# Kernel optimization log

Hardware: AMD Instinct MI355X
Metric: run time of the kernel (lower is better)

The kernel has to match this reference:

```python
import jax, jax.numpy as jnp
import numpy as np

EPS = 0.1

def _kernels():
    # torch: sobel = [[-0.5,0,0.5]]*3 (2D), repeated along depth -> [1,1,3,3,3]
    s = np.array([[-0.5, 0.0, 0.5]] * 3, dtype=np.float32)        # grad along W
    kx = np.tile(s[None, :, :], (3, 1, 1))                        # [3,3,3]
    ky = np.tile(s.T[None, :, :], (3, 1, 1))                      # grad along H
    kz = np.zeros((3, 3, 3), dtype=np.float32)
    kz[0, :, :] = -0.5
    kz[2, :, :] = 0.5                                             # grad along D
    # OIDHW, O=I=1 (channel=1 depthwise)
    return (jnp.asarray(kx)[None, None], jnp.asarray(ky)[None, None], jnp.asarray(kz)[None, None])

KX, KY, KZ = _kernels()

def _conv(x, k):
    return jax.lax.conv_general_dilated(
        x, k, window_strides=(1, 1, 1), padding='VALID',
        dimension_numbers=('NCDHW', 'OIDHW', 'NCDHW'))

def _grads(x):
    # ReplicationPad3d(1) == edge padding on D,H,W
    xp = jnp.pad(x, ((0, 0), (0, 0), (1, 1), (1, 1), (1, 1)), mode='edge')
    return _conv(xp, KX), _conv(xp, KY), _conv(xp, KZ)

def setup_inputs() -> dict:
    key = jax.random.key(0)
    k1, k2, k3 = jax.random.split(key, 3)
    shp = (1, 1, 192, 192, 192)
    return {
        'I': jax.random.normal(k1, shp, dtype=jnp.float32),
        'J': jax.random.normal(k2, shp, dtype=jnp.float32),
        'mask': jax.random.uniform(k3, shp, dtype=jnp.float32),
    }

def reference(I, J, mask):
    Ix, Iy, Iz = _grads(I)
    Jx, Jy, Jz = _grads(J)
    I_mag = Ix * Ix + Iy * Iy + Iz * Iz + EPS * EPS
    J_mag = Jx * Jx + Jy * Jy + Jz * Jz + EPS * EPS
    dot = Ix * Jx + Iy * Jy + Iz * Jz          # == sum over concat channel dim (C=1)
    ngf = (dot * dot) / (I_mag * J_mag)
    return jnp.mean((1.0 - ngf) * mask)
```

## Files before the change

kernel.cpp:

```cpp
#include <hip/hip_runtime.h>

#define NN 192
#define BZ 4
#define YC 8
#define NTHR (64 * BZ)


__device__ __forceinline__ void row_ab(float c0, float c1, float c2, int lane,
                                       float a[3], float b[3]) {
    float L = __shfl_up(c2, 1, 64);
    float R = __shfl_down(c0, 1, 64);
    if (lane == 0)  L = c0;
    if (lane == 63) R = c2;
    a[0] = c1 - L;
    a[1] = c2 - c0;
    a[2] = R - c1;
    b[0] = L + c0 + c1;
    b[1] = c0 + c1 + c2;
    b[2] = c1 + c2 + R;
}

__device__ __forceinline__ void fold_plane(const float3 r[3], int lane,
                                           float sa[3], float sb[3], float tb[3]) {
    float am[3], bm[3], a0[3], b0[3], ap[3], bp[3];
    row_ab(r[0].x, r[0].y, r[0].z, lane, am, bm);
    row_ab(r[1].x, r[1].y, r[1].z, lane, a0, b0);
    row_ab(r[2].x, r[2].y, r[2].z, lane, ap, bp);
#pragma unroll
    for (int i = 0; i < 3; ++i) {
        sa[i] = am[i] + a0[i] + ap[i];
        sb[i] = bm[i] + b0[i] + bp[i];
        tb[i] = bp[i] - bm[i];
    }
}

__device__ __forceinline__ void load_plane(const float* const base[6], int yrow,
                                           float3 rI[3], float3 rJ[3]) {
#pragma unroll
    for (int d = 0; d < 3; ++d) rI[d] = *reinterpret_cast<const float3*>(base[d] + yrow);
#pragma unroll
    for (int d = 0; d < 3; ++d) rJ[d] = *reinterpret_cast<const float3*>(base[3 + d] + yrow);
}

__global__ __launch_bounds__(NTHR, 2) void ngf_kernel(const float* __restrict__ I,
                                                      const float* __restrict__ J,
                                                      const float* __restrict__ M,
                                                      float* __restrict__ out) {
    const int lane = threadIdx.x;
    const int tz = threadIdx.y;
    const int xoff = lane * 3;
    const int z = blockIdx.y * BZ + tz;
    const int ybase = blockIdx.x * YC;

    const int gzm = (z == 0) ? 0 : z - 1;
    const int gzp = (z == NN - 1) ? (NN - 1) : z + 1;

    const float* base[6] = {
        I + gzm * NN * NN + xoff, I + z * NN * NN + xoff, I + gzp * NN * NN + xoff,
        J + gzm * NN * NN + xoff, J + z * NN * NN + xoff, J + gzp * NN * NN + xoff};
    const float* mbase = M + z * NN * NN + xoff;

    float sa[2][3][3], sb[2][3][3], tb[2][3][3];

    {
        float3 rI[3], rJ[3];
        load_plane(base, ((ybase == 0) ? 0 : (ybase - 1)) * NN, rI, rJ);
        fold_plane(rI, lane, sa[0][0], sb[0][0], tb[0][0]);
        fold_plane(rJ, lane, sa[1][0], sb[1][0], tb[1][0]);
        load_plane(base, ybase * NN, rI, rJ);
        fold_plane(rI, lane, sa[0][1], sb[0][1], tb[0][1]);
        fold_plane(rJ, lane, sa[1][1], sb[1][1], tb[1][1]);
    }

    float3 bI[2][3], bJ[2][3];
    load_plane(base, (ybase + 1) * NN, bI[0], bJ[0]);
    float3 mcur = *reinterpret_cast<const float3*>(mbase + ybase * NN);

    float acc = 0.0f;
#pragma unroll
    for (int yy = 0; yy < YC; ++yy) {
        const int cb = yy & 1, nb = cb ^ 1;

        float3 mnxt = mcur;
        if (yy < YC - 1) {
            int gy = ybase + yy + 2;
            gy = (gy > NN - 1) ? (NN - 1) : gy;
            load_plane(base, gy * NN, bI[nb], bJ[nb]);
            mnxt = *reinterpret_cast<const float3*>(mbase + (ybase + yy + 1) * NN);
        }

        const int sC = (yy + 2) % 3;
        fold_plane(bI[cb], lane, sa[0][sC], sb[0][sC], tb[0][sC]);
        fold_plane(bJ[cb], lane, sa[1][sC], sb[1][sC], tb[1][sC]);

        const int s0 = yy % 3, s1 = (yy + 1) % 3;
        const float mm[3] = {mcur.x, mcur.y, mcur.z};
#pragma unroll
        for (int i = 0; i < 3; ++i) {
            const float Ix = sa[0][s0][i] + sa[0][s1][i] + sa[0][sC][i];
            const float Iy = sb[0][sC][i] - sb[0][s0][i];
            const float Iz = tb[0][s0][i] + tb[0][s1][i] + tb[0][sC][i];
            const float Jx = sa[1][s0][i] + sa[1][s1][i] + sa[1][sC][i];
            const float Jy = sb[1][sC][i] - sb[1][s0][i];
            const float Jz = tb[1][s0][i] + tb[1][s1][i] + tb[1][sC][i];
            const float im = Ix * Ix + Iy * Iy + Iz * Iz + 0.04f;
            const float jm = Jx * Jx + Jy * Jy + Jz * Jz + 0.04f;
            const float dot = Ix * Jx + Iy * Jy + Iz * Jz;
            acc += (1.0f - dot * dot * __builtin_amdgcn_rcpf(im * jm)) * mm[i];
        }
        mcur = mnxt;
    }

    acc *= (1.0f / ((float)NN * (float)NN * (float)NN));
#pragma unroll
    for (int off = 32; off > 0; off >>= 1)
        acc += __shfl_down(acc, off, 64);

    __shared__ float red[NTHR / 64];
    const int flat = tz * 64 + lane;
    if ((flat & 63) == 0) red[flat >> 6] = acc;
    __syncthreads();
    if (flat == 0) {
        float s = 0.0f;
#pragma unroll
        for (int w = 0; w < NTHR / 64; ++w) s += red[w];
        atomicAdd(out, s);
    }
}

extern "C" void kernel_launch(void* const* d_in, const int* in_sizes, int n_in,
                              void* d_out, int out_size, void* d_ws, size_t ws_size,
                              hipStream_t stream) {
    const float* I = (const float*)d_in[0];
    const float* J = (const float*)d_in[1];
    const float* M = (const float*)d_in[2];
    float* out = (float*)d_out;

    hipMemsetAsync(d_out, 0, sizeof(float), stream);

    dim3 block(64, BZ);
    dim3 grid(NN / YC, NN / BZ);
    ngf_kernel<<<grid, block, 0, stream>>>(I, J, M, out);
}
```

Measured before the change: 118.4 us.

## Refactor separable gradient folding to shuffle depth-reduced sums and enlarge y chunk

Restructures the separable stencil so each plane first reduces along depth (sum and difference), then exchanges only those two partials across lanes. That cuts cross-lane shuffles from six per row-triple to four, and the x, y and z gradients are assembled from 5-wide S/D/T windows. It also raises the per-block y chunk from 8 to 12 rows, which amortizes halo reloads, and asks for occupancy of 3 blocks per CU. The larger windows and chunk raise register pressure, which could force spills under the tighter launch bound, and with YC=12 the grid has fewer blocks.

Result: slower. 121.7 us (+2.7%).

```diff
diff --git a/kernel.cpp b/kernel.cpp
--- a/kernel.cpp
+++ b/kernel.cpp
@@ -2,36 +2,26 @@
 
 #define NN 192
 #define BZ 4
-#define YC 8
+#define YC 12
 #define NTHR (64 * BZ)
 
 
-__device__ __forceinline__ void row_ab(float c0, float c1, float c2, int lane,
-                                       float a[3], float b[3]) {
-    float L = __shfl_up(c2, 1, 64);
-    float R = __shfl_down(c0, 1, 64);
-    if (lane == 0)  L = c0;
-    if (lane == 63) R = c2;
-    a[0] = c1 - L;
-    a[1] = c2 - c0;
-    a[2] = R - c1;
-    b[0] = L + c0 + c1;
-    b[1] = c0 + c1 + c2;
-    b[2] = c1 + c2 + R;
-}
-
-__device__ __forceinline__ void fold_plane(const float3 r[3], int lane,
-                                           float sa[3], float sb[3], float tb[3]) {
-    float am[3], bm[3], a0[3], b0[3], ap[3], bp[3];
-    row_ab(r[0].x, r[0].y, r[0].z, lane, am, bm);
-    row_ab(r[1].x, r[1].y, r[1].z, lane, a0, b0);
-    row_ab(r[2].x, r[2].y, r[2].z, lane, ap, bp);
-#pragma unroll
-    for (int i = 0; i < 3; ++i) {
-        sa[i] = am[i] + a0[i] + ap[i];
-        sb[i] = bm[i] + b0[i] + bp[i];
-        tb[i] = bp[i] - bm[i];
-    }
+__device__ __forceinline__ void fold_pq(const float3 rm, const float3 r0, const float3 rp,
+                                        int lane, float pe[5], float qe[5]) {
+    const float p0 = rm.x + r0.x + rp.x;
+    const float p1 = rm.y + r0.y + rp.y;
+    const float p2 = rm.z + r0.z + rp.z;
+    const float q0 = rp.x - rm.x;
+    const float q1 = rp.y - rm.y;
+    const float q2 = rp.z - rm.z;
+    float pL = __shfl_up(p2, 1, 64);
+    float pR = __shfl_down(p0, 1, 64);
+    float qL = __shfl_up(q2, 1, 64);
+    float qR = __shfl_down(q0, 1, 64);
+    if (lane == 0)  { pL = p0; qL = q0; }
+    if (lane == 63) { pR = p2; qR = q2; }
+    pe[0] = pL; pe[1] = p0; pe[2] = p1; pe[3] = p2; pe[4] = pR;
+    qe[0] = qL; qe[1] = q0; qe[2] = q1; qe[3] = q2; qe[4] = qR;
 }
 
 __device__ __forceinline__ void load_plane(const float* const base[6], int yrow,
@@ -42,7 +32,7 @@
     for (int d = 0; d < 3; ++d) rJ[d] = *reinterpret_cast<const float3*>(base[3 + d] + yrow);
 }
 
-__global__ __launch_bounds__(NTHR, 2) void ngf_kernel(const float* __restrict__ I,
+__global__ __launch_bounds__(NTHR, 3) void ngf_kernel(const float* __restrict__ I,
                                                       const float* __restrict__ J,
                                                       const float* __restrict__ M,
                                                       float* __restrict__ out) {
@@ -60,16 +50,16 @@
         J + gzm * NN * NN + xoff, J + z * NN * NN + xoff, J + gzp * NN * NN + xoff};
     const float* mbase = M + z * NN * NN + xoff;
 
-    float sa[2][3][3], sb[2][3][3], tb[2][3][3];
+    float pe[2][3][5], qe[2][3][5];
 
     {
         float3 rI[3], rJ[3];
         load_plane(base, ((ybase == 0) ? 0 : (ybase - 1)) * NN, rI, rJ);
-        fold_plane(rI, lane, sa[0][0], sb[0][0], tb[0][0]);
-        fold_plane(rJ, lane, sa[1][0], sb[1][0], tb[1][0]);
+        fold_pq(rI[0], rI[1], rI[2], lane, pe[0][0], qe[0][0]);
+        fold_pq(rJ[0], rJ[1], rJ[2], lane, pe[1][0], qe[1][0]);
         load_plane(base, ybase * NN, rI, rJ);
-        fold_plane(rI, lane, sa[0][1], sb[0][1], tb[0][1]);
-        fold_plane(rJ, lane, sa[1][1], sb[1][1], tb[1][1]);
+        fold_pq(rI[0], rI[1], rI[2], lane, pe[0][1], qe[0][1]);
+        fold_pq(rJ[0], rJ[1], rJ[2], lane, pe[1][1], qe[1][1]);
     }
 
     float3 bI[2][3], bJ[2][3];
@@ -90,19 +80,32 @@
         }
 
         const int sC = (yy + 2) % 3;
-        fold_plane(bI[cb], lane, sa[0][sC], sb[0][sC], tb[0][sC]);
-        fold_plane(bJ[cb], lane, sa[1][sC], sb[1][sC], tb[1][sC]);
+        fold_pq(bI[cb][0], bI[cb][1], bI[cb][2], lane, pe[0][sC], qe[0][sC]);
+        fold_pq(bJ[cb][0], bJ[cb][1], bJ[cb][2], lane, pe[1][sC], qe[1][sC]);
 
         const int s0 = yy % 3, s1 = (yy + 1) % 3;
+        float G[2][3][3];
+#pragma unroll
+        for (int ar = 0; ar < 2; ++ar) {
+            float S[5], D[5], T[5];
+#pragma unroll
+            for (int i = 0; i < 5; ++i) {
+                S[i] = pe[ar][s0][i] + pe[ar][s1][i] + pe[ar][sC][i];
+                D[i] = pe[ar][sC][i] - pe[ar][s0][i];
+                T[i] = qe[ar][s0][i] + qe[ar][s1][i] + qe[ar][sC][i];
+            }
+#pragma unroll
+            for (int i = 0; i < 3; ++i) {
+                G[ar][0][i] = S[i + 2] - S[i];
+                G[ar][1][i] = D[i] + D[i + 1] + D[i + 2];
+                G[ar][2][i] = T[i] + T[i + 1] + T[i + 2];
+            }
+        }
         const float mm[3] = {mcur.x, mcur.y, mcur.z};
 #pragma unroll
         for (int i = 0; i < 3; ++i) {
-            const float Ix = sa[0][s0][i] + sa[0][s1][i] + sa[0][sC][i];
-            const float Iy = sb[0][sC][i] - sb[0][s0][i];
-            const float Iz = tb[0][s0][i] + tb[0][s1][i] + tb[0][sC][i];
-            const float Jx = sa[1][s0][i] + sa[1][s1][i] + sa[1][sC][i];
-            const float Jy = sb[1][sC][i] - sb[1][s0][i];
-            const float Jz = tb[1][s0][i] + tb[1][s1][i] + tb[1][sC][i];
+            const float Ix = G[0][0][i], Iy = G[0][1][i], Iz = G[0][2][i];
+            const float Jx = G[1][0][i], Jy = G[1][1][i], Jz = G[1][2][i];
             const float im = Ix * Ix + Iy * Iy + Iz * Iz + 0.04f;
             const float jm = Jx * Jx + Jy * Jy + Jz * Jz + 0.04f;
             const float dot = Ix * Jx + Iy * Jy + Iz * Jz;
```
